# Kernel tuning notes

Hardware: AMD Instinct MI355X
Metric: run time of the kernel (lower is better)

The kernel has to match this reference:

```python
import jax, jax.numpy as jnp
import numpy as np
import math

B, S, D, H = 1, 2048, 1024, 16
HD = D // H  # 64
SCALE = 1.0 / math.sqrt(HD)
ENT = 0.5      # entanglement_strength
DECAY = 0.1    # correlation_decay
SUP = 0.3      # superposition_weight
EPS = 1e-5


def setup_inputs() -> dict:
    key = jax.random.key(0)
    ks = jax.random.split(key, 24)
    def w(k, shape, s=0.02):
        return jax.random.normal(k, shape, dtype=jnp.float32) * s
    return {
        "hidden_states": jax.random.normal(ks[0], (B, S, D), dtype=jnp.float32),
        "Wq": w(ks[1], (D, D)), "bq": jnp.zeros((D,), jnp.float32),
        "Wk": w(ks[2], (D, D)), "bk": jnp.zeros((D,), jnp.float32),
        "Wv": w(ks[3], (D, D)), "bv": jnp.zeros((D,), jnp.float32),
        "Wo": w(ks[4], (D, D)), "bo": jnp.zeros((D,), jnp.float32),
        "Weq": w(ks[5], (D, D), 0.002), "beq": jnp.zeros((D,), jnp.float32),
        "Wek": w(ks[6], (D, D), 0.002), "bek": jnp.zeros((D,), jnp.float32),
        "amp_w": w(ks[7], (H, D)), "amp_b": jnp.zeros((H,), jnp.float32),
        "ph_w": w(ks[8], (H, D)), "ph_b": jnp.zeros((H,), jnp.float32),
        "mix_w": w(ks[9], (H, HD, HD)), "mix_b": jnp.zeros((H, HD), jnp.float32),
        "ln_g": jnp.ones((D,), jnp.float32), "ln_b": jnp.zeros((D,), jnp.float32),
    }


def _heads(x):
    # [B,S,D] -> [B,H,S,hd]
    b, s, _ = x.shape
    return x.reshape(b, s, H, HD).transpose(0, 2, 1, 3)


def reference(hidden_states, Wq, bq, Wk, bk, Wv, bv, Wo, bo,
              Weq, beq, Wek, bek, amp_w, amp_b, ph_w, ph_b,
              mix_w, mix_b, ln_g, ln_b):
    hs = hidden_states
    b, s, _ = hs.shape
    q = _heads(hs @ Wq.T + bq)  # [B,H,S,hd]
    k = _heads(hs @ Wk.T + bk)
    v = _heads(hs @ Wv.T + bv)

    # standard attention scores
    scores = jnp.einsum('bhqd,bhkd->bhqk', q, k) * SCALE

    # entanglement scores with distance-decay position bias
    eq = _heads(hs @ Weq.T + beq)
    ek = _heads(hs @ Wek.T + bek)
    pos = jnp.arange(s)
    decay = jnp.exp(-DECAY * jnp.abs(pos[:, None] - pos[None, :]).astype(jnp.float32))  # [S,S]
    esc = jnp.einsum('bhqd,bhkd->bhqk', eq, ek) * (1.0 / math.sqrt(HD)) * decay

    attn = jax.nn.softmax(scores + ENT * esc, axis=-1)  # [B,H,S,S]

    # quantum amplitudes / phases
    amps = jax.nn.sigmoid(hs @ amp_w.T + amp_b)        # [B,S,H]
    phases = jnp.tanh(hs @ ph_w.T + ph_b) * math.pi    # [B,S,H]
    a = amps.transpose(0, 2, 1)[..., None]             # [B,H,S,1]
    p = phases.transpose(0, 2, 1)[..., None]

    # per-head superposition mixer: Linear(head_dim, head_dim) per head
    sup = jnp.einsum('bhsd,hod->bhso', v, mix_w) + mix_b[None, :, None, :]
    mixed = v + SUP * a * jnp.cos(p) * sup + SUP * a * jnp.sin(p) * jnp.roll(sup, 1, axis=-1)

    ctx = jnp.einsum('bhqk,bhkd->bhqd', attn, mixed)
    ctx = ctx.transpose(0, 2, 1, 3).reshape(b, s, D)
    out = ctx @ Wo.T + bo

    # residual + LayerNorm
    res = hs + out
    mu = jnp.mean(res, axis=-1, keepdims=True)
    var = jnp.mean((res - mu) ** 2, axis=-1, keepdims=True)
    return (res - mu) * jax.lax.rsqrt(var + EPS) * ln_g + ln_b
```

## Files before the change

kernel.cpp:

```cpp
#include <hip/hip_runtime.h>

#define SEQ 2048
#define DM  1024
#define NH  16
#define HDIM 64

typedef __bf16   bf16x8 __attribute__((ext_vector_type(8)));
typedef float    f32x4  __attribute__((ext_vector_type(4)));
typedef _Float16 half8  __attribute__((ext_vector_type(8)));
typedef _Float16 half4v __attribute__((ext_vector_type(4)));

__global__ void zero_out(float* __restrict__ out, int n) {
    int i = blockIdx.x * 256 + threadIdx.x;
    if (i < n) out[i] = 0.f;
}

__global__ __launch_bounds__(256) void cvt_bf16(
    const float* __restrict__ src, __bf16* __restrict__ dst, int n8)
{
    int i = blockIdx.x * 256 + threadIdx.x;
    if (i >= n8) return;
    const float4* s = reinterpret_cast<const float4*>(src) + (size_t)i * 2;
    float4 x = s[0], y = s[1];
    bf16x8 o;
    o[0] = (__bf16)x.x; o[1] = (__bf16)x.y; o[2] = (__bf16)x.z; o[3] = (__bf16)x.w;
    o[4] = (__bf16)y.x; o[5] = (__bf16)y.y; o[6] = (__bf16)y.z; o[7] = (__bf16)y.w;
    reinterpret_cast<bf16x8*>(dst)[i] = o;
}

struct CvtBatch { const float* src[6]; __bf16* dst[6]; };
__global__ __launch_bounds__(256) void cvt_w6(CvtBatch cb) {
    const int z = blockIdx.y;
    int i = blockIdx.x * 256 + threadIdx.x;
    const float4* s = reinterpret_cast<const float4*>(cb.src[z]) + (size_t)i * 2;
    float4 x = s[0], y = s[1];
    bf16x8 o;
    o[0] = (__bf16)x.x; o[1] = (__bf16)x.y; o[2] = (__bf16)x.z; o[3] = (__bf16)x.w;
    o[4] = (__bf16)y.x; o[5] = (__bf16)y.y; o[6] = (__bf16)y.z; o[7] = (__bf16)y.w;
    reinterpret_cast<bf16x8*>(cb.dst[z])[i] = o;
}

__global__ __launch_bounds__(256) void wsup_k(
    const float* __restrict__ mixw, const float* __restrict__ Wv,
    const float* __restrict__ bv, const float* __restrict__ mixb,
    __bf16* __restrict__ w6, float* __restrict__ bsup)
{
    const int ho = blockIdx.x, h = ho >> 6, tid = threadIdx.x;
    __shared__ float mrow[64];
    if (tid < 64) mrow[tid] = mixw[(size_t)ho * 64 + tid];
    __syncthreads();
    const int c0 = tid * 4;
    float a0 = 0.f, a1 = 0.f, a2 = 0.f, a3 = 0.f;
    for (int dd = 0; dd < 64; ++dd) {
        const float4 wv4 = *reinterpret_cast<const float4*>(
            Wv + (size_t)(h * 64 + dd) * DM + c0);
        const float w = mrow[dd];
        a0 += w * wv4.x; a1 += w * wv4.y; a2 += w * wv4.z; a3 += w * wv4.w;
    }
    __bf16* dst = w6 + (size_t)ho * DM + c0;
    dst[0] = (__bf16)a0; dst[1] = (__bf16)a1; dst[2] = (__bf16)a2; dst[3] = (__bf16)a3;
    if (tid == 0) {
        float b = mixb[ho];
        for (int dd = 0; dd < 64; ++dd) b += mrow[dd] * bv[h * 64 + dd];
        bsup[ho] = b;
    }
}

struct GemmBatch {
    const __bf16* A;
    const __bf16* W[6];
    const float*  bias[6];
    void*         out[6];
    int           mode[6];
    const float*  resid;
};

__device__ __forceinline__ int swz4(int r) { return (r ^ (r >> 2)) & 3; }

__global__ __launch_bounds__(256) void gemm_bt(GemmBatch g) {
    const int z = blockIdx.z;
    const __bf16* __restrict__ A = g.A;
    const __bf16* __restrict__ W = g.W[z];
    const int ncol0 = blockIdx.x * 128;
    const int mrow0 = blockIdx.y * 128;
    const int tid = threadIdx.x, lane = tid & 63, wv = tid >> 6;
    const int wm = wv >> 1, wn = wv & 1;
    const int fr = lane & 15, fj = lane >> 4;

    __shared__ __bf16 As[128 * 32];
    __shared__ __bf16 Bs[128 * 32];

    f32x4 acc[4][4];
#pragma unroll
    for (int i = 0; i < 4; ++i)
#pragma unroll
        for (int j = 0; j < 4; ++j)
#pragma unroll
            for (int e = 0; e < 4; ++e) acc[i][j][e] = 0.f;

    const int c0 = tid, c1 = tid + 256;
    const int r0 = c0 >> 2, j0 = c0 & 3;
    const int r1 = c1 >> 2, j1 = c1 & 3;
    const int la0 = r0 * 32 + ((j0 ^ swz4(r0)) << 3);
    const int la1 = r1 * 32 + ((j1 ^ swz4(r1)) << 3);

    const __bf16* Ap0 = A + (size_t)(mrow0 + r0) * DM + j0 * 8;
    const __bf16* Ap1 = A + (size_t)(mrow0 + r1) * DM + j1 * 8;
    const __bf16* Wp0 = W + (size_t)(ncol0 + r0) * DM + j0 * 8;
    const __bf16* Wp1 = W + (size_t)(ncol0 + r1) * DM + j1 * 8;

    bf16x8 ra0 = *(const bf16x8*)(Ap0);
    bf16x8 ra1 = *(const bf16x8*)(Ap1);
    bf16x8 rb0 = *(const bf16x8*)(Wp0);
    bf16x8 rb1 = *(const bf16x8*)(Wp1);

    for (int kt = 0; kt < DM; kt += 32) {
        __syncthreads();
        *(bf16x8*)(As + la0) = ra0;
        *(bf16x8*)(As + la1) = ra1;
        *(bf16x8*)(Bs + la0) = rb0;
        *(bf16x8*)(Bs + la1) = rb1;
        __syncthreads();
        if (kt + 32 < DM) {
            ra0 = *(const bf16x8*)(Ap0 + kt + 32);
            ra1 = *(const bf16x8*)(Ap1 + kt + 32);
            rb0 = *(const bf16x8*)(Wp0 + kt + 32);
            rb1 = *(const bf16x8*)(Wp1 + kt + 32);
        }
        bf16x8 af[4], bfv[4];
#pragma unroll
        for (int mf = 0; mf < 4; ++mf) {
            int r = wm * 64 + mf * 16 + fr;
            af[mf] = *(const bf16x8*)(As + r * 32 + ((fj ^ swz4(r)) << 3));
        }
#pragma unroll
        for (int nf = 0; nf < 4; ++nf) {
            int r = wn * 64 + nf * 16 + fr;
            bfv[nf] = *(const bf16x8*)(Bs + r * 32 + ((fj ^ swz4(r)) << 3));
        }
#pragma unroll
        for (int mf = 0; mf < 4; ++mf)
#pragma unroll
            for (int nf = 0; nf < 4; ++nf)
                acc[mf][nf] = __builtin_amdgcn_mfma_f32_16x16x32_bf16(
                    af[mf], bfv[nf], acc[mf][nf], 0, 0, 0);
    }

    const int mode = g.mode[z];
    const float* __restrict__ bias = g.bias[z];
#pragma unroll
    for (int mf = 0; mf < 4; ++mf) {
#pragma unroll
        for (int nf = 0; nf < 4; ++nf) {
            const int col = ncol0 + wn * 64 + nf * 16 + fr;
            const int rw0 = mrow0 + wm * 64 + mf * 16 + fj * 4;
            const float bc = bias[col];
#pragma unroll
            for (int jj = 0; jj < 4; ++jj) {
                float vv = acc[mf][nf][jj] + bc;
                const size_t idx = (size_t)(rw0 + jj) * DM + col;
                if (mode == 3) {
                    ((_Float16*)g.out[z])[idx] = (_Float16)vv;
                } else {
                    if (mode == 2) vv += g.resid[idx];
                    ((float*)g.out[z])[idx] = vv;
                }
            }
        }
    }
}

__global__ __launch_bounds__(256) void amp_fast(
    const float* __restrict__ hs,
    const float* __restrict__ amp_w, const float* __restrict__ amp_b,
    const float* __restrict__ ph_w,  const float* __restrict__ ph_b,
    float* __restrict__ cA, float* __restrict__ sA)
{
    const int s = blockIdx.x;
    __shared__ float hrow[DM];
    for (int i = threadIdx.x; i < DM; i += 256)
        hrow[i] = hs[(size_t)s * DM + i];
    __syncthreads();
    const int h = threadIdx.x >> 4, sub = threadIdx.x & 15;
    const float* aw = amp_w + (size_t)h * DM;
    const float* pw = ph_w  + (size_t)h * DM;
    float da = 0.f, dp = 0.f;
    for (int k = sub; k < DM; k += 16) {
        const float hv = hrow[k];
        da += hv * aw[k];
        dp += hv * pw[k];
    }
#pragma unroll
    for (int off = 8; off >= 1; off >>= 1) {
        da += __shfl_xor(da, off);
        dp += __shfl_xor(dp, off);
    }
    if (sub == 0) {
        da += amp_b[h]; dp += ph_b[h];
        float amp = 1.f / (1.f + expf(-da));
        float ph  = tanhf(dp) * 3.14159265358979323846f;
        cA[s * NH + h] = 0.3f * amp * cosf(ph);
        sA[s * NH + h] = 0.3f * amp * sinf(ph);
    }
}

__global__ __launch_bounds__(256) void mixT_fuse(
    const _Float16* __restrict__ vb, const _Float16* __restrict__ supf,
    const float* __restrict__ cA, const float* __restrict__ sA,
    _Float16* __restrict__ mixedT)
{
    const int h = blockIdx.x, st = blockIdx.y;
    const int o = threadIdx.x >> 2, sc = threadIdx.x & 3;
    const int s0 = st * 32 + sc * 8;
    const int ho = h * 64 + o, op = h * 64 + ((o + 63) & 63);
    half8 m;
#pragma unroll
    for (int e = 0; e < 8; ++e) {
        const int s = s0 + e;
        const float v  = (float)vb[(size_t)s * DM + ho];
        const float su = (float)supf[(size_t)s * DM + ho];
        const float s2 = (float)supf[(size_t)s * DM + op];
        m[e] = (_Float16)(v + cA[s * NH + h] * su + sA[s * NH + h] * s2);
    }
    *reinterpret_cast<half8*>(mixedT + (size_t)ho * SEQ + s0) = m;
}

__global__ __launch_bounds__(256) void attn_mfma(
    const _Float16* __restrict__ q, const _Float16* __restrict__ k,
    const _Float16* __restrict__ eq, const _Float16* __restrict__ ek,
    const _Float16* __restrict__ mixedT, __bf16* __restrict__ ctx)
{
    const int h = blockIdx.y;
    const int q0 = blockIdx.x * 64;
    const int tid = threadIdx.x, lane = tid & 63, wv = tid >> 6;
    const int lo = lane & 15, hi = lane >> 4;
    const int hoff = h * HDIM;

    __shared__ _Float16 Kt[64 * 64];
    __shared__ _Float16 Et[64 * 64];
    __shared__ _Float16 Mt[64 * 64];
    __shared__ _Float16 Pt[4][64 * 18];

    half8 qa[2], ea[2];
#pragma unroll
    for (int kk = 0; kk < 2; ++kk) {
        const int row = q0 + wv * 16 + lo;
        qa[kk] = *(const half8*)(q  + (size_t)row * DM + hoff + kk * 32 + hi * 8);
        ea[kk] = *(const half8*)(eq + (size_t)row * DM + hoff + kk * 32 + hi * 8);
    }

    f32x4 oacc[4];
    float mr[4], lr[4];
#pragma unroll
    for (int j = 0; j < 4; ++j) { mr[j] = 0.f; lr[j] = 0.f; }
#pragma unroll
    for (int n = 0; n < 4; ++n)
#pragma unroll
        for (int e = 0; e < 4; ++e) oacc[n][e] = 0.f;

    const int srow = tid >> 3, schk = tid & 7;
    const int sdst0 = srow * 64 + ((schk ^ (srow & 7)) << 3);
    const int sdst1 = (srow + 32) * 64 + ((schk ^ (srow & 7)) << 3);

    half8 rk0 = *(const half8*)(k  + (size_t)(srow) * DM + hoff + schk * 8);
    half8 rk1 = *(const half8*)(k  + (size_t)(srow + 32) * DM + hoff + schk * 8);
    half8 re0 = *(const half8*)(ek + (size_t)(srow) * DM + hoff + schk * 8);
    half8 re1 = *(const half8*)(ek + (size_t)(srow + 32) * DM + hoff + schk * 8);
    half8 rm0 = *(const half8*)(mixedT + (size_t)(hoff + srow) * SEQ + schk * 8);
    half8 rm1 = *(const half8*)(mixedT + (size_t)(hoff + srow + 32) * SEQ + schk * 8);

    for (int kt = 0; kt < SEQ; kt += 64) {
        __syncthreads();
        *(half8*)&Kt[sdst0] = rk0; *(half8*)&Kt[sdst1] = rk1;
        *(half8*)&Et[sdst0] = re0; *(half8*)&Et[sdst1] = re1;
        *(half8*)&Mt[sdst0] = rm0; *(half8*)&Mt[sdst1] = rm1;
        __syncthreads();
        if (kt + 64 < SEQ) {
            const int nt = kt + 64;
            rk0 = *(const half8*)(k  + (size_t)(nt + srow) * DM + hoff + schk * 8);
            rk1 = *(const half8*)(k  + (size_t)(nt + srow + 32) * DM + hoff + schk * 8);
            re0 = *(const half8*)(ek + (size_t)(nt + srow) * DM + hoff + schk * 8);
            re1 = *(const half8*)(ek + (size_t)(nt + srow + 32) * DM + hoff + schk * 8);
            rm0 = *(const half8*)(mixedT + (size_t)(hoff + srow) * SEQ + nt + schk * 8);
            rm1 = *(const half8*)(mixedT + (size_t)(hoff + srow + 32) * SEQ + nt + schk * 8);
        }

        f32x4 sa[4], se[4];
#pragma unroll
        for (int n = 0; n < 4; ++n)
#pragma unroll
            for (int e = 0; e < 4; ++e) { sa[n][e] = 0.f; se[n][e] = 0.f; }
#pragma unroll
        for (int kk = 0; kk < 2; ++kk)
#pragma unroll
            for (int nf = 0; nf < 4; ++nf) {
                const int rrow = lo + 16 * nf;
                const int coff = rrow * 64 + (((hi + 4 * kk) ^ (rrow & 7)) << 3);
                half8 kb = *(const half8*)&Kt[coff];
                half8 eb = *(const half8*)&Et[coff];
                sa[nf] = __builtin_amdgcn_mfma_f32_16x16x32_f16(qa[kk], kb, sa[nf], 0, 0, 0);
                se[nf] = __builtin_amdgcn_mfma_f32_16x16x32_f16(ea[kk], eb, se[nf], 0, 0, 0);
            }

        float lg[4][4];
        bool exc = false;
        const int qrow = q0 + wv * 16 + hi * 4;
#pragma unroll
        for (int nf = 0; nf < 4; ++nf) {
            const int key = kt + nf * 16 + lo;
#pragma unroll
            for (int j = 0; j < 4; ++j) {
                int dd = qrow + j - key; dd = dd < 0 ? -dd : dd;
                const float dec = exp2f(-0.14426950408889634f * (float)dd);
                const float v = 0.125f * sa[nf][j] + 0.0625f * se[nf][j] * dec;
                lg[nf][j] = v;
                exc |= (v > mr[j] + 8.f);
            }
        }
        if (__any((int)exc)) {
#pragma unroll
            for (int j = 0; j < 4; ++j) {
                float tm = fmaxf(fmaxf(lg[0][j], lg[1][j]), fmaxf(lg[2][j], lg[3][j]));
#pragma unroll
                for (int off = 8; off >= 1; off >>= 1) tm = fmaxf(tm, __shfl_xor(tm, off));
                const float mnew = fmaxf(mr[j], tm);
                const float corr = expf(mr[j] - mnew);
                lr[j] *= corr; mr[j] = mnew;
#pragma unroll
                for (int nfd = 0; nfd < 4; ++nfd) oacc[nfd][j] *= corr;
            }
        }
        _Float16* Pw = Pt[wv];
#pragma unroll
        for (int nf = 0; nf < 4; ++nf) {
            half4v pv;
#pragma unroll
            for (int j = 0; j < 4; ++j) {
                const float p = expf(lg[nf][j] - mr[j]);
                lr[j] += p;
                pv[j] = (_Float16)p;
            }
            *(half4v*)&Pw[(lo + 16 * nf) * 18 + hi * 4] = pv;
        }
        __asm__ volatile("s_waitcnt lgkmcnt(0)" ::: "memory");

#pragma unroll
        for (int kk = 0; kk < 2; ++kk) {
            half8 mb[4];
#pragma unroll
            for (int nfd = 0; nfd < 4; ++nfd) {
                const int rrow = lo + 16 * nfd;
                mb[nfd] = *(const half8*)&Mt[rrow * 64 + (((hi + 4 * kk) ^ (rrow & 7)) << 3)];
            }
            half8 pa;
#pragma unroll
            for (int e = 0; e < 8; ++e)
                pa[e] = Pw[(kk * 32 + hi * 8 + e) * 18 + lo];
#pragma unroll
            for (int nfd = 0; nfd < 4; ++nfd)
                oacc[nfd] = __builtin_amdgcn_mfma_f32_16x16x32_f16(pa, mb[nfd], oacc[nfd], 0, 0, 0);
        }
    }

#pragma unroll
    for (int j = 0; j < 4; ++j) {
#pragma unroll
        for (int off = 8; off >= 1; off >>= 1) lr[j] += __shfl_xor(lr[j], off);
    }
    const int qrow = q0 + wv * 16 + hi * 4;
#pragma unroll
    for (int nfd = 0; nfd < 4; ++nfd) {
        const int d = hoff + lo + 16 * nfd;
#pragma unroll
        for (int j = 0; j < 4; ++j)
            ctx[(size_t)(qrow + j) * DM + d] = (__bf16)(oacc[nfd][j] / lr[j]);
    }
}

__global__ __launch_bounds__(256) void lnorm_f32(
    const float* __restrict__ res, const float* __restrict__ g,
    const float* __restrict__ b, float* __restrict__ out)
{
    const int row = blockIdx.x, tid = threadIdx.x;
    const int wave = tid >> 6, lane = tid & 63;
    __shared__ float red[8];
    const float4 x = reinterpret_cast<const float4*>(res + (size_t)row * DM)[tid];
    float s  = x.x + x.y + x.z + x.w;
    float s2 = x.x * x.x + x.y * x.y + x.z * x.z + x.w * x.w;
#pragma unroll
    for (int off = 32; off >= 1; off >>= 1) {
        s  += __shfl_xor(s, off);
        s2 += __shfl_xor(s2, off);
    }
    if (lane == 0) { red[wave] = s; red[4 + wave] = s2; }
    __syncthreads();
    s  = red[0] + red[1] + red[2] + red[3];
    s2 = red[4] + red[5] + red[6] + red[7];
    const float mu  = s * (1.f / DM);
    const float var = s2 * (1.f / DM) - mu * mu;
    const float inv = rsqrtf(var + 1e-5f);
    const int col = tid * 4;
    float4 o;
    o.x = (x.x - mu) * inv * g[col + 0] + b[col + 0];
    o.y = (x.y - mu) * inv * g[col + 1] + b[col + 1];
    o.z = (x.z - mu) * inv * g[col + 2] + b[col + 2];
    o.w = (x.w - mu) * inv * g[col + 3] + b[col + 3];
    reinterpret_cast<float4*>(out + (size_t)row * DM)[tid] = o;
}

extern "C" void kernel_launch(void* const* d_in, const int* in_sizes, int n_in,
                              void* d_out, int out_size, void* d_ws, size_t ws_size,
                              hipStream_t stream) {
    const float* hs   = (const float*)d_in[0];
    const float* Wq   = (const float*)d_in[1];
    const float* bq   = (const float*)d_in[2];
    const float* Wk   = (const float*)d_in[3];
    const float* bk   = (const float*)d_in[4];
    const float* Wv   = (const float*)d_in[5];
    const float* bv   = (const float*)d_in[6];
    const float* Wo   = (const float*)d_in[7];
    const float* bo   = (const float*)d_in[8];
    const float* Weq  = (const float*)d_in[9];
    const float* beq  = (const float*)d_in[10];
    const float* Wek  = (const float*)d_in[11];
    const float* bek  = (const float*)d_in[12];
    const float* ampw = (const float*)d_in[13];
    const float* ampb = (const float*)d_in[14];
    const float* phw  = (const float*)d_in[15];
    const float* phb  = (const float*)d_in[16];
    const float* mixw = (const float*)d_in[17];
    const float* mixb = (const float*)d_in[18];
    const float* lng  = (const float*)d_in[19];
    const float* lnb  = (const float*)d_in[20];
    float* out = (float*)d_out;

    static const int expect[21] = {
        2097152, 1048576, 1024, 1048576, 1024, 1048576, 1024, 1048576, 1024,
        1048576, 1024, 1048576, 1024, 16384, 16, 16384, 16, 65536, 1024,
        1024, 1024};
    bool ok = (n_in == 21) && (out_size == 2097152);
    if (ok) for (int i = 0; i < 21; ++i) ok = ok && (in_sizes[i] == expect[i]);
    if (!ok) {
        zero_out<<<(out_size + 255) / 256, 256, 0, stream>>>(out, out_size);
        return;
    }

    char* ws = (char*)d_ws;
    __bf16*   hsb = (__bf16*)ws;
    __bf16*   w0  = (__bf16*)(ws + (4  << 20));
    __bf16*   w1  = (__bf16*)(ws + (6  << 20));
    __bf16*   w2  = (__bf16*)(ws + (8  << 20));
    __bf16*   w3  = (__bf16*)(ws + (10 << 20));
    __bf16*   w4  = (__bf16*)(ws + (12 << 20));
    __bf16*   w5  = (__bf16*)(ws + (14 << 20));
    __bf16*   w6  = (__bf16*)(ws + (16 << 20));
    _Float16* qf  = (_Float16*)(ws + (18 << 20));
    _Float16* kf  = (_Float16*)(ws + (22 << 20));
    _Float16* eqf = (_Float16*)(ws + (26 << 20));
    _Float16* ekf = (_Float16*)(ws + (30 << 20));
    float*    cA  = (float*)(ws + (34 << 20));
    float*    sA  = cA + SEQ * NH;
    float*    bsup = sA + SEQ * NH;
    _Float16* mxT = (_Float16*)hsb;
    float*    res = (float*)(ws + (18 << 20));
    _Float16* vb   = (_Float16*)d_out;
    _Float16* supf = (_Float16*)((char*)d_out + (4 << 20));
    __bf16*   ctx  = (__bf16*)d_out;

    const int H8 = SEQ * DM / 8;
    cvt_bf16<<<(H8 + 255) / 256, 256, 0, stream>>>(hs, hsb, H8);

    CvtBatch cb;
    cb.src[0] = Wq;  cb.dst[0] = w0;
    cb.src[1] = Wk;  cb.dst[1] = w1;
    cb.src[2] = Wv;  cb.dst[2] = w2;
    cb.src[3] = Weq; cb.dst[3] = w3;
    cb.src[4] = Wek; cb.dst[4] = w4;
    cb.src[5] = Wo;  cb.dst[5] = w5;
    cvt_w6<<<dim3(512, 6), 256, 0, stream>>>(cb);

    wsup_k<<<1024, 256, 0, stream>>>(mixw, Wv, bv, mixb, w6, bsup);
    amp_fast<<<SEQ, 256, 0, stream>>>(hs, ampw, ampb, phw, phb, cA, sA);

    GemmBatch g1 = {};
    g1.A = hsb;
    g1.W[0] = w0; g1.bias[0] = bq;   g1.out[0] = qf;   g1.mode[0] = 3;
    g1.W[1] = w1; g1.bias[1] = bk;   g1.out[1] = kf;   g1.mode[1] = 3;
    g1.W[2] = w2; g1.bias[2] = bv;   g1.out[2] = vb;   g1.mode[2] = 3;
    g1.W[3] = w3; g1.bias[3] = beq;  g1.out[3] = eqf;  g1.mode[3] = 3;
    g1.W[4] = w4; g1.bias[4] = bek;  g1.out[4] = ekf;  g1.mode[4] = 3;
    g1.W[5] = w6; g1.bias[5] = bsup; g1.out[5] = supf; g1.mode[5] = 3;
    g1.resid = nullptr;
    gemm_bt<<<dim3(DM / 128, SEQ / 128, 6), 256, 0, stream>>>(g1);

    mixT_fuse<<<dim3(NH, SEQ / 32), 256, 0, stream>>>(vb, supf, cA, sA, mxT);

    attn_mfma<<<dim3(SEQ / 64, NH), 256, 0, stream>>>(qf, kf, eqf, ekf, mxT, ctx);

    GemmBatch g3 = {};
    g3.A = ctx;
    g3.W[0] = w5; g3.bias[0] = bo; g3.out[0] = res; g3.mode[0] = 2;
    g3.resid = hs;
    gemm_bt<<<dim3(DM / 128, SEQ / 128, 1), 256, 0, stream>>>(g3);

    lnorm_f32<<<SEQ, 256, 0, stream>>>(res, lng, lnb, out);
}
```

Baseline: 354.5 us.

## Skip entanglement score tiles outside decay band and use direct-to-LDS GEMM loads

In the attention kernel, entanglement-score MFMAs, ek loads and decay math now run only for key tiles within about 160 positions of the query tile. Outside that band the decay factor exp(-0.1*d) is treated as zero, which approximates the exact result under the assumption that the decay is negligible there. The projection GEMM now uses global_load_lds to copy tiles straight into shared memory, dropping the register prefetch so loads are no longer overlapped with compute. The softmax also switches expf to __expf.

```diff
diff --git a/kernel.cpp b/kernel.cpp
--- a/kernel.cpp
+++ b/kernel.cpp
@@ -9,6 +9,12 @@
 typedef float    f32x4  __attribute__((ext_vector_type(4)));
 typedef _Float16 half8  __attribute__((ext_vector_type(8)));
 typedef _Float16 half4v __attribute__((ext_vector_type(4)));
+
+__device__ __forceinline__ void gload16(const void* g, void* l) {
+    __builtin_amdgcn_global_load_lds(
+        (const __attribute__((address_space(1))) unsigned int*)g,
+        (__attribute__((address_space(3))) unsigned int*)l, 16, 0, 0);
+}
 
 __global__ void zero_out(float* __restrict__ out, int n) {
     int i = blockIdx.x * 256 + threadIdx.x;
@@ -98,35 +104,24 @@
 #pragma unroll
             for (int e = 0; e < 4; ++e) acc[i][j][e] = 0.f;
 
-    const int c0 = tid, c1 = tid + 256;
-    const int r0 = c0 >> 2, j0 = c0 & 3;
-    const int r1 = c1 >> 2, j1 = c1 & 3;
-    const int la0 = r0 * 32 + ((j0 ^ swz4(r0)) << 3);
-    const int la1 = r1 * 32 + ((j1 ^ swz4(r1)) << 3);
-
-    const __bf16* Ap0 = A + (size_t)(mrow0 + r0) * DM + j0 * 8;
-    const __bf16* Ap1 = A + (size_t)(mrow0 + r1) * DM + j1 * 8;
-    const __bf16* Wp0 = W + (size_t)(ncol0 + r0) * DM + j0 * 8;
-    const __bf16* Wp1 = W + (size_t)(ncol0 + r1) * DM + j1 * 8;
-
-    bf16x8 ra0 = *(const bf16x8*)(Ap0);
-    bf16x8 ra1 = *(const bf16x8*)(Ap1);
-    bf16x8 rb0 = *(const bf16x8*)(Wp0);
-    bf16x8 rb1 = *(const bf16x8*)(Wp1);
+    const int row0 = wv * 16 + (lane >> 2);
+    const int row1 = row0 + 64;
+    const int jl   = lane & 3;
+    const int dstA0 = row0 * 32 + jl * 8;
+    const int dstA1 = row1 * 32 + jl * 8;
+    const __bf16* ApS0 = A + (size_t)(mrow0 + row0) * DM + (jl ^ swz4(row0)) * 8;
+    const __bf16* ApS1 = A + (size_t)(mrow0 + row1) * DM + (jl ^ swz4(row1)) * 8;
+    const __bf16* WpS0 = W + (size_t)(ncol0 + row0) * DM + (jl ^ swz4(row0)) * 8;
+    const __bf16* WpS1 = W + (size_t)(ncol0 + row1) * DM + (jl ^ swz4(row1)) * 8;
 
     for (int kt = 0; kt < DM; kt += 32) {
         __syncthreads();
-        *(bf16x8*)(As + la0) = ra0;
-        *(bf16x8*)(As + la1) = ra1;
-        *(bf16x8*)(Bs + la0) = rb0;
-        *(bf16x8*)(Bs + la1) = rb1;
+        gload16(ApS0 + kt, As + dstA0);
+        gload16(ApS1 + kt, As + dstA1);
+        gload16(WpS0 + kt, Bs + dstA0);
+        gload16(WpS1 + kt, Bs + dstA1);
         __syncthreads();
-        if (kt + 32 < DM) {
-            ra0 = *(const bf16x8*)(Ap0 + kt + 32);
-            ra1 = *(const bf16x8*)(Ap1 + kt + 32);
-            rb0 = *(const bf16x8*)(Wp0 + kt + 32);
-            rb1 = *(const bf16x8*)(Wp1 + kt + 32);
-        }
+
         bf16x8 af[4], bfv[4];
 #pragma unroll
         for (int mf = 0; mf < 4; ++mf) {
@@ -262,27 +257,37 @@
     const int sdst0 = srow * 64 + ((schk ^ (srow & 7)) << 3);
     const int sdst1 = (srow + 32) * 64 + ((schk ^ (srow & 7)) << 3);
 
+    #define IN_BAND(kt_) ({ int _a = (kt_) - (q0 + 63); int _b = q0 - ((kt_) + 63); \
+                            int _d = _a > 0 ? _a : (_b > 0 ? _b : 0); _d <= 160; })
+
+    bool diagCur = IN_BAND(0);
     half8 rk0 = *(const half8*)(k  + (size_t)(srow) * DM + hoff + schk * 8);
     half8 rk1 = *(const half8*)(k  + (size_t)(srow + 32) * DM + hoff + schk * 8);
-    half8 re0 = *(const half8*)(ek + (size_t)(srow) * DM + hoff + schk * 8);
-    half8 re1 = *(const half8*)(ek + (size_t)(srow + 32) * DM + hoff + schk * 8);
     half8 rm0 = *(const half8*)(mixedT + (size_t)(hoff + srow) * SEQ + schk * 8);
     half8 rm1 = *(const half8*)(mixedT + (size_t)(hoff + srow + 32) * SEQ + schk * 8);
+    half8 re0, re1;
+    if (diagCur) {
+        re0 = *(const half8*)(ek + (size_t)(srow) * DM + hoff + schk * 8);
+        re1 = *(const half8*)(ek + (size_t)(srow + 32) * DM + hoff + schk * 8);
+    }
 
     for (int kt = 0; kt < SEQ; kt += 64) {
         __syncthreads();
         *(half8*)&Kt[sdst0] = rk0; *(half8*)&Kt[sdst1] = rk1;
-        *(half8*)&Et[sdst0] = re0; *(half8*)&Et[sdst1] = re1;
         *(half8*)&Mt[sdst0] = rm0; *(half8*)&Mt[sdst1] = rm1;
+        if (diagCur) { *(half8*)&Et[sdst0] = re0; *(half8*)&Et[sdst1] = re1; }
         __syncthreads();
+        const bool diagNext = (kt + 64 < SEQ) && IN_BAND(kt + 64);
         if (kt + 64 < SEQ) {
             const int nt = kt + 64;
             rk0 = *(const half8*)(k  + (size_t)(nt + srow) * DM + hoff + schk * 8);
             rk1 = *(const half8*)(k  + (size_t)(nt + srow + 32) * DM + hoff + schk * 8);
-            re0 = *(const half8*)(ek + (size_t)(nt + srow) * DM + hoff + schk * 8);
-            re1 = *(const half8*)(ek + (size_t)(nt + srow + 32) * DM + hoff + schk * 8);
             rm0 = *(const half8*)(mixedT + (size_t)(hoff + srow) * SEQ + nt + schk * 8);
             rm1 = *(const half8*)(mixedT + (size_t)(hoff + srow + 32) * SEQ + nt + schk * 8);
+            if (diagNext) {
+                re0 = *(const half8*)(ek + (size_t)(nt + srow) * DM + hoff + schk * 8);
+                re1 = *(const half8*)(ek + (size_t)(nt + srow + 32) * DM + hoff + schk * 8);
+            }
         }
 
         f32x4 sa[4], se[4];
@@ -297,25 +302,45 @@
                 const int rrow = lo + 16 * nf;
                 const int coff = rrow * 64 + (((hi + 4 * kk) ^ (rrow & 7)) << 3);
                 half8 kb = *(const half8*)&Kt[coff];
-                half8 eb = *(const half8*)&Et[coff];
                 sa[nf] = __builtin_amdgcn_mfma_f32_16x16x32_f16(qa[kk], kb, sa[nf], 0, 0, 0);
-                se[nf] = __builtin_amdgcn_mfma_f32_16x16x32_f16(ea[kk], eb, se[nf], 0, 0, 0);
-            }
+            }
+        if (diagCur) {
+#pragma unroll
+            for (int kk = 0; kk < 2; ++kk)
+#pragma unroll
+                for (int nf = 0; nf < 4; ++nf) {
+                    const int rrow = lo + 16 * nf;
+                    const int coff = rrow * 64 + (((hi + 4 * kk) ^ (rrow & 7)) << 3);
+                    half8 eb = *(const half8*)&Et[coff];
+                    se[nf] = __builtin_amdgcn_mfma_f32_16x16x32_f16(ea[kk], eb, se[nf], 0, 0, 0);
+                }
+        }
 
         float lg[4][4];
         bool exc = false;
         const int qrow = q0 + wv * 16 + hi * 4;
-#pragma unroll
-        for (int nf = 0; nf < 4; ++nf) {
-            const int key = kt + nf * 16 + lo;
-#pragma unroll
-            for (int j = 0; j < 4; ++j) {
-                int dd = qrow + j - key; dd = dd < 0 ? -dd : dd;
-                const float dec = exp2f(-0.14426950408889634f * (float)dd);
-                const float v = 0.125f * sa[nf][j] + 0.0625f * se[nf][j] * dec;
-                lg[nf][j] = v;
-                exc |= (v > mr[j] + 8.f);
-            }
+        if (diagCur) {
+#pragma unroll
+            for (int nf = 0; nf < 4; ++nf) {
+                const int key = kt + nf * 16 + lo;
+#pragma unroll
+                for (int j = 0; j < 4; ++j) {
+                    int dd = qrow + j - key; dd = dd < 0 ? -dd : dd;
+                    const float dec = exp2f(-0.14426950408889634f * (float)dd);
+                    const float v = 0.125f * sa[nf][j] + 0.0625f * se[nf][j] * dec;
+                    lg[nf][j] = v;
+                    exc |= (v > mr[j] + 8.f);
+                }
+            }
+        } else {
+#pragma unroll
+            for (int nf = 0; nf < 4; ++nf)
+#pragma unroll
+                for (int j = 0; j < 4; ++j) {
+                    const float v = 0.125f * sa[nf][j];
+                    lg[nf][j] = v;
+                    exc |= (v > mr[j] + 8.f);
+                }
         }
         if (__any((int)exc)) {
 #pragma unroll
@@ -324,7 +349,7 @@
 #pragma unroll
                 for (int off = 8; off >= 1; off >>= 1) tm = fmaxf(tm, __shfl_xor(tm, off));
                 const float mnew = fmaxf(mr[j], tm);
-                const float corr = expf(mr[j] - mnew);
+                const float corr = __expf(mr[j] - mnew);
                 lr[j] *= corr; mr[j] = mnew;
 #pragma unroll
                 for (int nfd = 0; nfd < 4; ++nfd) oacc[nfd][j] *= corr;
@@ -336,7 +361,7 @@
             half4v pv;
 #pragma unroll
             for (int j = 0; j < 4; ++j) {
-                const float p = expf(lg[nf][j] - mr[j]);
+                const float p = __expf(lg[nf][j] - mr[j]);
                 lr[j] += p;
                 pv[j] = (_Float16)p;
             }
@@ -360,7 +385,9 @@
             for (int nfd = 0; nfd < 4; ++nfd)
                 oacc[nfd] = __builtin_amdgcn_mfma_f32_16x16x32_f16(pa, mb[nfd], oacc[nfd], 0, 0, 0);
         }
-    }
+        diagCur = diagNext;
+    }
+    #undef IN_BAND
 
 #pragma unroll
     for (int j = 0; j < 4; ++j) {
```

New measurement: 303.6 us. -14.4%, faster.
